# Performance work log

Hardware: AMD Instinct MI355X
Metric: run time of the kernel (lower is better)

The kernel has to match this reference:

```python
import jax, jax.numpy as jnp
import numpy as np

N = 50000        # nodes
E = 1600000      # edges (before self-loops)
F_IN = 11        # QM9 node features
H = 128          # dim_h
G = 1024         # number of graphs in the mega-batch
T = 1            # targets_num


def setup_inputs() -> dict:
    key = jax.random.key(0)
    ks = jax.random.split(key, 8)
    x = jax.random.normal(ks[0], (N, F_IN), jnp.float32)
    edge_index = jax.random.randint(ks[1], (2, E), 0, N, dtype=jnp.int32)
    batch = jnp.sort(jax.random.randint(ks[2], (N,), 0, G, dtype=jnp.int32))
    W1 = jax.random.normal(ks[3], (F_IN, H), jnp.float32) / np.float32(np.sqrt(F_IN))
    b1 = jnp.zeros((H,), jnp.float32)
    W2 = jax.random.normal(ks[4], (H, H), jnp.float32) / np.float32(np.sqrt(H))
    b2 = jnp.zeros((H,), jnp.float32)
    W3 = jax.random.normal(ks[5], (H, H), jnp.float32) / np.float32(np.sqrt(H))
    b3 = jnp.zeros((H,), jnp.float32)
    Wl = jax.random.normal(ks[6], (H, T), jnp.float32) / np.float32(np.sqrt(H))
    bl = jnp.zeros((T,), jnp.float32)
    return {"x": x, "edge_index": edge_index, "batch": batch,
            "W1": W1, "b1": b1, "W2": W2, "b2": b2, "W3": W3, "b3": b3,
            "Wl": Wl, "bl": bl}


def gcn_conv(x, W, b, src, dst, norm, n):
    # PyG GCNConv: linear (no bias), normalized scatter-add over edges, then bias.
    h = x @ W                                  # [N, H]
    msg = h[src] * norm[:, None]               # [E+N, H] gather + scale
    agg = jax.ops.segment_sum(msg, dst, num_segments=n)
    return agg + b


def reference(x, edge_index, batch, W1, b1, W2, b2, W3, b3, Wl, bl):
    n = x.shape[0]
    loop = jnp.arange(n, dtype=edge_index.dtype)
    src = jnp.concatenate([edge_index[0], loop])   # self-loops added (PyG default)
    dst = jnp.concatenate([edge_index[1], loop])
    deg = jax.ops.segment_sum(jnp.ones_like(dst, jnp.float32), dst, num_segments=n)
    dinv = jnp.where(deg > 0, jax.lax.rsqrt(jnp.maximum(deg, 1.0)), 0.0)
    norm = dinv[src] * dinv[dst]                   # D^{-1/2}(A+I)D^{-1/2}

    h = jax.nn.relu(gcn_conv(x, W1, b1, src, dst, norm, n))
    h = jax.nn.relu(gcn_conv(h, W2, b2, src, dst, norm, n))
    h = gcn_conv(h, W3, b3, src, dst, norm, n)

    # global mean pool over graph segment ids
    g = batch.astype(jnp.int32)
    s = jax.ops.segment_sum(h, g, num_segments=G)
    cnt = jax.ops.segment_sum(jnp.ones((n, 1), jnp.float32), g, num_segments=G)
    pooled = s / jnp.maximum(cnt, 1.0)

    # dropout is identity at eval time (training=False)
    return pooled @ Wl + bl
```

## Files before the change

### kernel.cpp

```cpp
#include <hip/hip_runtime.h>
#include <hip/hip_fp16.h>


constexpr int N_NODES = 50000;
constexpr int N_EDGES = 1600000;
constexpr int F_IN_C  = 11;
constexpr int HC      = 128;
constexpr int G_C     = 1024;
constexpr int NPB     = 128;
constexpr int NB      = (N_NODES + NPB - 1) / NPB;
constexpr int CHUNK   = 8192;
constexpr int NBLK_E  = (N_EDGES + CHUNK - 1) / CHUNK;
constexpr int ZROW    = N_NODES;
constexpr int GM      = 32;


__device__ __forceinline__ unsigned pack_f16(float x, float y) {
  __half2 h = __floats2half2_rn(x, y);
  return *reinterpret_cast<unsigned*>(&h);
}

__device__ __forceinline__ float2 unpack_f16(unsigned u) {
  __half2 h = *reinterpret_cast<__half2*>(&u);
  return __half22float2(h);
}


__global__ __launch_bounds__(256) void k_bhist(const int* __restrict__ dst,
                                               int* __restrict__ bcnt) {
  __shared__ int hist[NB];
  int t = threadIdx.x;
  for (int b = t; b < NB; b += 256) hist[b] = 0;
  __syncthreads();
  long e0 = (long)blockIdx.x * CHUNK;
  for (int it = 0; it < CHUNK / 1024; ++it) {
    long e = e0 + it * 1024 + t * 4;
    if (e < N_EDGES) {
      int4 d4 = *(const int4*)(dst + e);
      atomicAdd(&hist[d4.x >> 7], 1);
      atomicAdd(&hist[d4.y >> 7], 1);
      atomicAdd(&hist[d4.z >> 7], 1);
      atomicAdd(&hist[d4.w >> 7], 1);
    }
  }
  __syncthreads();
  for (int b = t; b < NB; b += 256)
    if (hist[b]) atomicAdd(&bcnt[b], hist[b]);
}

__global__ __launch_bounds__(512) void k_prefix(const int* __restrict__ bcnt,
                                                int* __restrict__ bbase,
                                                int* __restrict__ bcur) {
  __shared__ int sc[512];
  int t = threadIdx.x;
  int v = (t < NB) ? bcnt[t] : 0;
  sc[t] = v;
  __syncthreads();
  for (int off = 1; off < 512; off <<= 1) {
    int a = (t >= off) ? sc[t - off] : 0;
    __syncthreads();
    sc[t] += a;
    __syncthreads();
  }
  if (t < NB) {
    int excl = sc[t] - v;
    bbase[t] = excl;
    bcur[t]  = excl;
  }
}

__global__ __launch_bounds__(256) void k_bin(const int* __restrict__ src,
                                             const int* __restrict__ dst,
                                             int* __restrict__ bcur,
                                             unsigned int* __restrict__ pairs) {
  __shared__ int hist[NB], base[NB], loff[NB];
  int t = threadIdx.x;
  for (int b = t; b < NB; b += 256) { hist[b] = 0; loff[b] = 0; }
  __syncthreads();
  long e0 = (long)blockIdx.x * CHUNK;
  for (int it = 0; it < CHUNK / 1024; ++it) {
    long e = e0 + it * 1024 + t * 4;
    if (e < N_EDGES) {
      int4 d4 = *(const int4*)(dst + e);
      atomicAdd(&hist[d4.x >> 7], 1);
      atomicAdd(&hist[d4.y >> 7], 1);
      atomicAdd(&hist[d4.z >> 7], 1);
      atomicAdd(&hist[d4.w >> 7], 1);
    }
  }
  __syncthreads();
  for (int b = t; b < NB; b += 256)
    if (hist[b]) base[b] = atomicAdd(&bcur[b], hist[b]);
  __syncthreads();
  for (int it = 0; it < CHUNK / 1024; ++it) {
    long e = e0 + it * 1024 + t * 4;
    if (e < N_EDGES) {
      int4 s4 = *(const int4*)(src + e);
      int4 d4 = *(const int4*)(dst + e);
      {
        int b = d4.x >> 7;
        int l = atomicAdd(&loff[b], 1);
        pairs[base[b] + l] = (unsigned)s4.x | ((unsigned)(d4.x & 127) << 16);
      }
      {
        int b = d4.y >> 7;
        int l = atomicAdd(&loff[b], 1);
        pairs[base[b] + l] = (unsigned)s4.y | ((unsigned)(d4.y & 127) << 16);
      }
      {
        int b = d4.z >> 7;
        int l = atomicAdd(&loff[b], 1);
        pairs[base[b] + l] = (unsigned)s4.z | ((unsigned)(d4.z & 127) << 16);
      }
      {
        int b = d4.w >> 7;
        int l = atomicAdd(&loff[b], 1);
        pairs[base[b] + l] = (unsigned)s4.w | ((unsigned)(d4.w & 127) << 16);
      }
    }
  }
}

__global__ __launch_bounds__(256) void k_build(const unsigned int* __restrict__ pairs,
                                               const int* __restrict__ bbase,
                                               const int* __restrict__ bcur,
                                               int* __restrict__ total,
                                               int* __restrict__ start,
                                               int* __restrict__ deg,
                                               float* __restrict__ dinv,
                                               int* __restrict__ csr) {
  __shared__ int cntL[NPB], sc[NPB];
  __shared__ int csrBaseL;
  int t = threadIdx.x;
  int b = blockIdx.x;
  int nodeBase = b * NPB;
  int nib = min(NPB, N_NODES - nodeBase);
  int pbase = bbase[b];
  int pend  = bcur[b];
  int size  = pend - pbase;
  if (t < NPB) cntL[t] = 0;
  __syncthreads();
  for (int p = t; p < size; p += 256)
    atomicAdd(&cntL[pairs[pbase + p] >> 16], 1);
  __syncthreads();
  int d = 0, dpad = 0;
  if (t < NPB && t < nib) {
    d = cntL[t] + 1;
    dpad = (d + 7) & ~7;
  }
  if (t < NPB) sc[t] = dpad;
  __syncthreads();
  for (int off = 1; off < NPB; off <<= 1) {
    int a = 0;
    if (t < NPB && t >= off) a = sc[t - off];
    __syncthreads();
    if (t < NPB) sc[t] += a;
    __syncthreads();
  }
  if (t == 0) csrBaseL = atomicAdd(total, sc[NPB - 1]);
  __syncthreads();
  int csrBase = csrBaseL;
  if (t < nib) {
    int excl = sc[t] - dpad;
    int n = nodeBase + t;
    int s = csrBase + excl;
    start[n] = s;
    deg[n]   = dpad;
    dinv[n]  = rsqrtf((float)d);
    csr[s]   = n;
    for (int k = d; k < dpad; ++k) csr[s + k] = ZROW;
    cntL[t]  = excl + 1;
  }
  __syncthreads();
  for (int p = t; p < size; p += 256) {
    unsigned v = pairs[pbase + p];
    int loc = atomicAdd(&cntL[v >> 16], 1);
    csr[csrBase + loc] = (int)(v & 0xFFFFu);
  }
}


__global__ __launch_bounds__(256) void k_lin1(const float* __restrict__ x,
                                              const float* __restrict__ W1,
                                              const float* __restrict__ dinv,
                                              unsigned* __restrict__ out) {
  __shared__ float w_s[F_IN_C * HC];
  for (int i = threadIdx.x; i < F_IN_C * HC; i += 256) w_s[i] = W1[i];
  __syncthreads();
  int lane = threadIdx.x & 63;
  int sub  = threadIdx.x >> 6;
  for (int n = blockIdx.x * 4 + sub; n < N_NODES; n += gridDim.x * 4) {
    const float* xr = x + (size_t)n * F_IN_C;
    float ax = 0.f, ay = 0.f;
#pragma unroll
    for (int k = 0; k < F_IN_C; ++k) {
      float xv = xr[k];
      ax += xv * w_s[k * HC + 2 * lane];
      ay += xv * w_s[k * HC + 2 * lane + 1];
    }
    float dn = dinv[n];
    out[(size_t)n * 64 + lane] = pack_f16(ax * dn, ay * dn);
  }
}

__global__ __launch_bounds__(128) void k_gemm(const float* __restrict__ in,
                                              const float* __restrict__ W,
                                              const float* __restrict__ dinv,
                                              unsigned* __restrict__ out) {
  __shared__ float in_s[GM][HC];
  int t  = threadIdx.x;
  int n0 = blockIdx.x * GM;
  int rows = min(GM, N_NODES - n0);
  const float4* inv4 = (const float4*)(in + (size_t)n0 * HC);
  float4* s4 = (float4*)&in_s[0][0];
  if (rows == GM) {
#pragma unroll
    for (int r = 0; r < 8; ++r) s4[t + r * 128] = inv4[t + r * 128];
  } else {
#pragma unroll
    for (int r = 0; r < 8; ++r) {
      int fv = t + r * 128;
      s4[fv] = (fv / 32 < rows) ? inv4[fv] : make_float4(0.f, 0.f, 0.f, 0.f);
    }
  }
  __syncthreads();
  int tp = t & 31;
  int rg = t >> 5;
  float a0[8], a1[8], a2[8], a3[8];
#pragma unroll
  for (int r = 0; r < 8; ++r) { a0[r] = 0.f; a1[r] = 0.f; a2[r] = 0.f; a3[r] = 0.f; }
  for (int k = 0; k < HC; ++k) {
    float4 w4 = *(const float4*)(W + k * HC + 4 * tp);
#pragma unroll
    for (int r = 0; r < 8; ++r) {
      float a = in_s[rg * 8 + r][k];
      a0[r] += a * w4.x;
      a1[r] += a * w4.y;
      a2[r] += a * w4.z;
      a3[r] += a * w4.w;
    }
  }
#pragma unroll
  for (int r = 0; r < 8; ++r) {
    int n = n0 + rg * 8 + r;
    if (n < N_NODES) {
      float dn = dinv[n];
      uint2 pk;
      pk.x = pack_f16(a0[r] * dn, a1[r] * dn);
      pk.y = pack_f16(a2[r] * dn, a3[r] * dn);
      *(uint2*)&out[(size_t)n * 64 + 2 * tp] = pk;
    }
  }
}

__global__ __launch_bounds__(128) void k_v3(const float* __restrict__ W3,
                                            const float* __restrict__ b3,
                                            const float* __restrict__ Wl,
                                            float* __restrict__ v3,
                                            float* __restrict__ c3,
                                            unsigned* __restrict__ lin1,
                                            unsigned* __restrict__ lin2,
                                            float* __restrict__ tbuf) {
  int k = threadIdx.x;
  float acc = 0.f;
  for (int j = 0; j < HC; ++j) acc += W3[k * HC + j] * Wl[j];
  v3[k] = acc;
  if (k < 64) {
    lin1[(size_t)ZROW * 64 + k] = 0u;
    lin2[(size_t)ZROW * 64 + k] = 0u;
  }
  if (k == 64) tbuf[ZROW] = 0.f;
  __shared__ float red[128];
  red[k] = b3[k] * Wl[k];
  __syncthreads();
  for (int s = 64; s > 0; s >>= 1) {
    if (k < s) red[k] += red[k + s];
    __syncthreads();
  }
  if (k == 0) *c3 = red[0];
}


template <int MODE>
__global__ __launch_bounds__(256) void k_spmm(const unsigned* __restrict__ lin,
                                              const float* __restrict__ dinv,
                                              const int* __restrict__ start,
                                              const int* __restrict__ deg,
                                              const int* __restrict__ csr,
                                              const float* __restrict__ bias,
                                              const float* __restrict__ v3,
                                              float* __restrict__ out) {
  int wv = threadIdx.x >> 6, lane = threadIdx.x & 63;
  int n = blockIdx.x * 4 + wv;
  if (n >= N_NODES) return;
  int s0 = start[n], d = deg[n];
  float dn = dinv[n];
  const unsigned* lp = lin + lane;
  float ax[8], ay[8];
#pragma unroll
  for (int u = 0; u < 8; ++u) { ax[u] = 0.f; ay[u] = 0.f; }
  int nb = d >> 3;
  int4 cc0 = *(const int4*)(csr + s0);
  int4 cc1 = *(const int4*)(csr + s0 + 4);
  unsigned qA[8];
  qA[0] = lp[(size_t)cc0.x * 64];
  qA[1] = lp[(size_t)cc0.y * 64];
  qA[2] = lp[(size_t)cc0.z * 64];
  qA[3] = lp[(size_t)cc0.w * 64];
  qA[4] = lp[(size_t)cc1.x * 64];
  qA[5] = lp[(size_t)cc1.y * 64];
  qA[6] = lp[(size_t)cc1.z * 64];
  qA[7] = lp[(size_t)cc1.w * 64];
  if (nb > 1) {
    cc0 = *(const int4*)(csr + s0 + 8);
    cc1 = *(const int4*)(csr + s0 + 12);
  }
  for (int b = 1; b < nb; ++b) {
    unsigned qB[8];
    qB[0] = lp[(size_t)cc0.x * 64];
    qB[1] = lp[(size_t)cc0.y * 64];
    qB[2] = lp[(size_t)cc0.z * 64];
    qB[3] = lp[(size_t)cc0.w * 64];
    qB[4] = lp[(size_t)cc1.x * 64];
    qB[5] = lp[(size_t)cc1.y * 64];
    qB[6] = lp[(size_t)cc1.z * 64];
    qB[7] = lp[(size_t)cc1.w * 64];
    if (b + 1 < nb) {
      cc0 = *(const int4*)(csr + s0 + (b + 1) * 8);
      cc1 = *(const int4*)(csr + s0 + (b + 1) * 8 + 4);
    }
#pragma unroll
    for (int u = 0; u < 8; ++u) {
      float2 v = unpack_f16(qA[u]);
      ax[u] += v.x;
      ay[u] += v.y;
    }
#pragma unroll
    for (int u = 0; u < 8; ++u) qA[u] = qB[u];
  }
#pragma unroll
  for (int u = 0; u < 8; ++u) {
    float2 v = unpack_f16(qA[u]);
    ax[u] += v.x;
    ay[u] += v.y;
  }
  float sx = ((ax[0] + ax[1]) + (ax[2] + ax[3])) + ((ax[4] + ax[5]) + (ax[6] + ax[7]));
  float sy = ((ay[0] + ay[1]) + (ay[2] + ay[3])) + ((ay[4] + ay[5]) + (ay[6] + ay[7]));
  sx = fmaxf(sx * dn + bias[lane * 2], 0.f);
  sy = fmaxf(sy * dn + bias[lane * 2 + 1], 0.f);
  if (MODE == 0) {
    ((float2*)out)[(size_t)n * 64 + lane] = make_float2(sx, sy);
  } else {
    float2 vv = ((const float2*)v3)[lane];
    float p = sx * vv.x + sy * vv.y;
#pragma unroll
    for (int o = 32; o > 0; o >>= 1) p += __shfl_down(p, o, 64);
    if (lane == 0) out[n] = p * dn;
  }
}

__global__ __launch_bounds__(256) void k_spmv_pool(const float* __restrict__ t,
                                                   const float* __restrict__ dinv,
                                                   const int* __restrict__ start,
                                                   const int* __restrict__ deg,
                                                   const int* __restrict__ csr,
                                                   const float* __restrict__ c3,
                                                   const int* __restrict__ batch,
                                                   float* __restrict__ ssum,
                                                   int* __restrict__ cntg) {
  int n = blockIdx.x * 256 + threadIdx.x;
  if (n >= N_NODES) return;
  int s0 = start[n], d = deg[n];
  float a0 = 0.f, a1 = 0.f, a2 = 0.f, a3 = 0.f;
  for (int i = 0; i + 4 <= d; i += 4) {
    int4 c = *(const int4*)(csr + s0 + i);
    a0 += t[c.x];
    a1 += t[c.y];
    a2 += t[c.z];
    a3 += t[c.w];
  }
  float acc = ((a0 + a1) + (a2 + a3)) * dinv[n] + *c3;
  int g = batch[n];
  atomicAdd(&ssum[g], acc);
  atomicAdd(&cntg[g], 1);
}

__global__ __launch_bounds__(256) void k_out(const float* __restrict__ ssum,
                                             const int* __restrict__ cntg,
                                             const float* __restrict__ bl,
                                             float* __restrict__ out) {
  int g = blockIdx.x * 256 + threadIdx.x;
  if (g < G_C) out[g] = ssum[g] / fmaxf((float)cntg[g], 1.f) + bl[0];
}


extern "C" void kernel_launch(void* const* d_in, const int* in_sizes, int n_in,
                              void* d_out, int out_size, void* d_ws, size_t ws_size,
                              hipStream_t stream) {
  const float* x     = (const float*)d_in[0];
  const int*   ei    = (const int*)d_in[1];
  const int*   srcE  = ei;
  const int*   dstE  = ei + N_EDGES;
  const int*   batch = (const int*)d_in[2];
  const float* W1 = (const float*)d_in[3];
  const float* b1 = (const float*)d_in[4];
  const float* W2 = (const float*)d_in[5];
  const float* b2 = (const float*)d_in[6];
  const float* W3 = (const float*)d_in[7];
  const float* b3 = (const float*)d_in[8];
  const float* Wl = (const float*)d_in[9];
  const float* bl = (const float*)d_in[10];
  float* out = (float*)d_out;

  size_t off = 0;
  auto alloc = [&](size_t bytes) -> char* {
    char* p = (char*)d_ws + off;
    off = (off + bytes + 15) & ~(size_t)15;
    return p;
  };
  char* bufA = alloc((size_t)(N_NODES + 1) * 2 * 256);
  float* bufB = (float*)alloc((size_t)N_NODES * HC * 4);
  unsigned* pairs = (unsigned*)bufA;
  unsigned* lin1  = (unsigned*)bufA;
  unsigned* lin2  = (unsigned*)(bufA + (size_t)(N_NODES + 1) * 256);
  float* dinv = (float*)alloc((size_t)N_NODES * 4);
  float* tbuf = (float*)alloc((size_t)(N_NODES + 1) * 4);
  float* v3   = (float*)alloc(HC * 4);
  float* c3   = (float*)alloc(16);
  int* startA = (int*)alloc((size_t)N_NODES * 4);
  int* degA   = (int*)alloc((size_t)N_NODES * 4);
  int* csr    = (int*)alloc((size_t)(N_EDGES + 8 * N_NODES) * 4);
  int* bbase  = (int*)alloc(NB * 4);
  int* bcur   = (int*)alloc(NB * 4);
  size_t zz_bytes = NB * 4 + 16 + G_C * 4 + G_C * 4;
  char* zz = alloc(zz_bytes);
  int*   bcnt = (int*)zz;
  int*   total= (int*)(zz + NB * 4);
  float* ssum = (float*)(zz + NB * 4 + 16);
  int*   cntg = (int*)(zz + NB * 4 + 16 + G_C * 4);

  hipMemsetAsync(zz, 0, zz_bytes, stream);

  k_bhist<<<NBLK_E, 256, 0, stream>>>(dstE, bcnt);
  k_prefix<<<1, 512, 0, stream>>>(bcnt, bbase, bcur);
  k_bin<<<NBLK_E, 256, 0, stream>>>(srcE, dstE, bcur, pairs);
  k_build<<<NB, 256, 0, stream>>>(pairs, bbase, bcur, total, startA, degA, dinv, csr);
  k_v3<<<1, 128, 0, stream>>>(W3, b3, Wl, v3, c3, lin1, lin2, tbuf);

  k_lin1<<<N_NODES / 4, 256, 0, stream>>>(x, W1, dinv, lin1);
  k_spmm<0><<<N_NODES / 4, 256, 0, stream>>>(lin1, dinv, startA, degA, csr, b1, v3, bufB);
  k_gemm<<<(N_NODES + GM - 1) / GM, 128, 0, stream>>>(bufB, W2, dinv, lin2);
  k_spmm<1><<<N_NODES / 4, 256, 0, stream>>>(lin2, dinv, startA, degA, csr, b2, v3, tbuf);
  k_spmv_pool<<<(N_NODES + 255) / 256, 256, 0, stream>>>(tbuf, dinv, startA, degA, csr,
                                                         c3, batch, ssum, cntg);
  k_out<<<(G_C + 255) / 256, 256, 0, stream>>>(ssum, cntg, bl, out);
}
```

Baseline: 241.1 us.

## Bin edges by source tile and destination block to localize CSR neighbor order

```diff
diff --git a/kernel.cpp b/kernel.cpp
--- a/kernel.cpp
+++ b/kernel.cpp
@@ -9,10 +9,14 @@
 constexpr int G_C     = 1024;
 constexpr int NPB     = 128;
 constexpr int NB      = (N_NODES + NPB - 1) / NPB;
+constexpr int TSH     = 13;
+constexpr int NT      = (N_NODES + (1 << TSH) - 1) >> TSH;
+constexpr int NBINS   = NT * NB;
 constexpr int CHUNK   = 8192;
 constexpr int NBLK_E  = (N_EDGES + CHUNK - 1) / CHUNK;
 constexpr int ZROW    = N_NODES;
 constexpr int GM      = 32;
+constexpr int EPL     = (NBINS + 63) / 64;
 
 
 __device__ __forceinline__ unsigned pack_f16(float x, float y) {
@@ -26,46 +30,57 @@
 }
 
 
-__global__ __launch_bounds__(256) void k_bhist(const int* __restrict__ dst,
+__device__ __forceinline__ int bin_of(int s, int d) {
+  return (s >> TSH) * NB + (d >> 7);
+}
+
+__global__ __launch_bounds__(256) void k_bhist(const int* __restrict__ src,
+                                               const int* __restrict__ dst,
                                                int* __restrict__ bcnt) {
-  __shared__ int hist[NB];
+  __shared__ int hist[NBINS];
   int t = threadIdx.x;
-  for (int b = t; b < NB; b += 256) hist[b] = 0;
+  for (int b = t; b < NBINS; b += 256) hist[b] = 0;
   __syncthreads();
   long e0 = (long)blockIdx.x * CHUNK;
   for (int it = 0; it < CHUNK / 1024; ++it) {
     long e = e0 + it * 1024 + t * 4;
     if (e < N_EDGES) {
+      int4 s4 = *(const int4*)(src + e);
       int4 d4 = *(const int4*)(dst + e);
-      atomicAdd(&hist[d4.x >> 7], 1);
-      atomicAdd(&hist[d4.y >> 7], 1);
-      atomicAdd(&hist[d4.z >> 7], 1);
-      atomicAdd(&hist[d4.w >> 7], 1);
-    }
-  }
-  __syncthreads();
-  for (int b = t; b < NB; b += 256)
+      atomicAdd(&hist[bin_of(s4.x, d4.x)], 1);
+      atomicAdd(&hist[bin_of(s4.y, d4.y)], 1);
+      atomicAdd(&hist[bin_of(s4.z, d4.z)], 1);
+      atomicAdd(&hist[bin_of(s4.w, d4.w)], 1);
+    }
+  }
+  __syncthreads();
+  for (int b = t; b < NBINS; b += 256)
     if (hist[b]) atomicAdd(&bcnt[b], hist[b]);
 }
 
-__global__ __launch_bounds__(512) void k_prefix(const int* __restrict__ bcnt,
-                                                int* __restrict__ bbase,
-                                                int* __restrict__ bcur) {
-  __shared__ int sc[512];
-  int t = threadIdx.x;
-  int v = (t < NB) ? bcnt[t] : 0;
-  sc[t] = v;
-  __syncthreads();
-  for (int off = 1; off < 512; off <<= 1) {
-    int a = (t >= off) ? sc[t - off] : 0;
-    __syncthreads();
-    sc[t] += a;
-    __syncthreads();
-  }
-  if (t < NB) {
-    int excl = sc[t] - v;
-    bbase[t] = excl;
-    bcur[t]  = excl;
+__global__ __launch_bounds__(64) void k_prefix(const int* __restrict__ bcnt,
+                                               int* __restrict__ bbase,
+                                               int* __restrict__ bcur) {
+  __shared__ int part[64];
+  int l = threadIdx.x;
+  int base = l * EPL;
+  int s = 0;
+  for (int i = 0; i < EPL; ++i)
+    if (base + i < NBINS) s += bcnt[base + i];
+  part[l] = s;
+  __syncthreads();
+  if (l == 0) {
+    int acc = 0;
+    for (int i = 0; i < 64; ++i) { int v = part[i]; part[i] = acc; acc += v; }
+  }
+  __syncthreads();
+  int run = part[l];
+  for (int i = 0; i < EPL; ++i) {
+    if (base + i < NBINS) {
+      bbase[base + i] = run;
+      bcur[base + i]  = run;
+      run += bcnt[base + i];
+    }
   }
 }
 
@@ -73,24 +88,26 @@
                                              const int* __restrict__ dst,
                                              int* __restrict__ bcur,
                                              unsigned int* __restrict__ pairs) {
-  __shared__ int hist[NB], base[NB], loff[NB];
+  __shared__ int hist[NBINS];
+  __shared__ int curL[NBINS];
   int t = threadIdx.x;
-  for (int b = t; b < NB; b += 256) { hist[b] = 0; loff[b] = 0; }
+  for (int b = t; b < NBINS; b += 256) hist[b] = 0;
   __syncthreads();
   long e0 = (long)blockIdx.x * CHUNK;
   for (int it = 0; it < CHUNK / 1024; ++it) {
     long e = e0 + it * 1024 + t * 4;
     if (e < N_EDGES) {
+      int4 s4 = *(const int4*)(src + e);
       int4 d4 = *(const int4*)(dst + e);
-      atomicAdd(&hist[d4.x >> 7], 1);
-      atomicAdd(&hist[d4.y >> 7], 1);
-      atomicAdd(&hist[d4.z >> 7], 1);
-      atomicAdd(&hist[d4.w >> 7], 1);
-    }
-  }
-  __syncthreads();
-  for (int b = t; b < NB; b += 256)
-    if (hist[b]) base[b] = atomicAdd(&bcur[b], hist[b]);
+      atomicAdd(&hist[bin_of(s4.x, d4.x)], 1);
+      atomicAdd(&hist[bin_of(s4.y, d4.y)], 1);
+      atomicAdd(&hist[bin_of(s4.z, d4.z)], 1);
+      atomicAdd(&hist[bin_of(s4.w, d4.w)], 1);
+    }
+  }
+  __syncthreads();
+  for (int b = t; b < NBINS; b += 256)
+    curL[b] = hist[b] ? atomicAdd(&bcur[b], hist[b]) : 0;
   __syncthreads();
   for (int it = 0; it < CHUNK / 1024; ++it) {
     long e = e0 + it * 1024 + t * 4;
@@ -98,24 +115,20 @@
       int4 s4 = *(const int4*)(src + e);
       int4 d4 = *(const int4*)(dst + e);
       {
-        int b = d4.x >> 7;
-        int l = atomicAdd(&loff[b], 1);
-        pairs[base[b] + l] = (unsigned)s4.x | ((unsigned)(d4.x & 127) << 16);
+        int p = atomicAdd(&curL[bin_of(s4.x, d4.x)], 1);
+        pairs[p] = (unsigned)s4.x | ((unsigned)(d4.x & 127) << 16);
       }
       {
-        int b = d4.y >> 7;
-        int l = atomicAdd(&loff[b], 1);
-        pairs[base[b] + l] = (unsigned)s4.y | ((unsigned)(d4.y & 127) << 16);
+        int p = atomicAdd(&curL[bin_of(s4.y, d4.y)], 1);
+        pairs[p] = (unsigned)s4.y | ((unsigned)(d4.y & 127) << 16);
       }
       {
-        int b = d4.z >> 7;
-        int l = atomicAdd(&loff[b], 1);
-        pairs[base[b] + l] = (unsigned)s4.z | ((unsigned)(d4.z & 127) << 16);
+        int p = atomicAdd(&curL[bin_of(s4.z, d4.z)], 1);
+        pairs[p] = (unsigned)s4.z | ((unsigned)(d4.z & 127) << 16);
       }
       {
-        int b = d4.w >> 7;
-        int l = atomicAdd(&loff[b], 1);
-        pairs[base[b] + l] = (unsigned)s4.w | ((unsigned)(d4.w & 127) << 16);
+        int p = atomicAdd(&curL[bin_of(s4.w, d4.w)], 1);
+        pairs[p] = (unsigned)s4.w | ((unsigned)(d4.w & 127) << 16);
       }
     }
   }
@@ -135,13 +148,14 @@
   int b = blockIdx.x;
   int nodeBase = b * NPB;
   int nib = min(NPB, N_NODES - nodeBase);
-  int pbase = bbase[b];
-  int pend  = bcur[b];
-  int size  = pend - pbase;
   if (t < NPB) cntL[t] = 0;
   __syncthreads();
-  for (int p = t; p < size; p += 256)
-    atomicAdd(&cntL[pairs[pbase + p] >> 16], 1);
+  for (int r = 0; r < NT; ++r) {
+    int pbase = bbase[r * NB + b];
+    int size  = bcur[r * NB + b] - pbase;
+    for (int p = t; p < size; p += 256)
+      atomicAdd(&cntL[pairs[pbase + p] >> 16], 1);
+  }
   __syncthreads();
   int d = 0, dpad = 0;
   if (t < NPB && t < nib) {
@@ -172,10 +186,15 @@
     cntL[t]  = excl + 1;
   }
   __syncthreads();
-  for (int p = t; p < size; p += 256) {
-    unsigned v = pairs[pbase + p];
-    int loc = atomicAdd(&cntL[v >> 16], 1);
-    csr[csrBase + loc] = (int)(v & 0xFFFFu);
+  for (int r = 0; r < NT; ++r) {
+    int pbase = bbase[r * NB + b];
+    int size  = bcur[r * NB + b] - pbase;
+    for (int p = t; p < size; p += 256) {
+      unsigned v = pairs[pbase + p];
+      int loc = atomicAdd(&cntL[v >> 16], 1);
+      csr[csrBase + loc] = (int)(v & 0xFFFFu);
+    }
+    __syncthreads();
   }
 }
 
@@ -430,19 +449,19 @@
   int* startA = (int*)alloc((size_t)N_NODES * 4);
   int* degA   = (int*)alloc((size_t)N_NODES * 4);
   int* csr    = (int*)alloc((size_t)(N_EDGES + 8 * N_NODES) * 4);
-  int* bbase  = (int*)alloc(NB * 4);
-  int* bcur   = (int*)alloc(NB * 4);
-  size_t zz_bytes = NB * 4 + 16 + G_C * 4 + G_C * 4;
+  int* bbase  = (int*)alloc(NBINS * 4);
+  int* bcur   = (int*)alloc(NBINS * 4);
+  size_t zz_bytes = NBINS * 4 + 16 + G_C * 4 + G_C * 4;
   char* zz = alloc(zz_bytes);
   int*   bcnt = (int*)zz;
-  int*   total= (int*)(zz + NB * 4);
-  float* ssum = (float*)(zz + NB * 4 + 16);
-  int*   cntg = (int*)(zz + NB * 4 + 16 + G_C * 4);
+  int*   total= (int*)(zz + NBINS * 4);
+  float* ssum = (float*)(zz + NBINS * 4 + 16);
+  int*   cntg = (int*)(zz + NBINS * 4 + 16 + G_C * 4);
 
   hipMemsetAsync(zz, 0, zz_bytes, stream);
 
-  k_bhist<<<NBLK_E, 256, 0, stream>>>(dstE, bcnt);
-  k_prefix<<<1, 512, 0, stream>>>(bcnt, bbase, bcur);
+  k_bhist<<<NBLK_E, 256, 0, stream>>>(srcE, dstE, bcnt);
+  k_prefix<<<1, 64, 0, stream>>>(bcnt, bbase, bcur);
   k_bin<<<NBLK_E, 256, 0, stream>>>(srcE, dstE, bcur, pairs);
   k_build<<<NB, 256, 0, stream>>>(pairs, bbase, bcur, total, startA, degA, dinv, csr);
   k_v3<<<1, 128, 0, stream>>>(W3, b3, Wl, v3, c3, lin1, lin2, tbuf);
```

Result: slower. 267.8 us (+11.1%).
